# Kernel optimization log

Measured on AMD Instinct MI355X. Metric: run time of the kernel, lower is better.

Reference implementation:

```python
import jax, jax.numpy as jnp
import numpy as np

H = 4      # num_heads
C = 64     # attention_num_c
C_Z = 128  # num_in_c (pair rep channels)
C_T = 64   # num_in_c_kv (template pair channels)


def setup_inputs() -> dict:
    key = jax.random.key(0)
    ks = jax.random.split(key, 7)
    B, T, R = 1, 4, 384
    z2d = jax.random.normal(ks[0], (B, R, R, C_Z), dtype=jnp.float32)
    t2d = jax.random.normal(ks[1], (B, T, R, R, C_T), dtype=jnp.float32)
    s = 0.02
    Wq = jax.random.normal(ks[2], (C_Z, H * C), dtype=jnp.float32) * s
    Wk = jax.random.normal(ks[3], (C_T, H * C), dtype=jnp.float32) * s
    Wv = jax.random.normal(ks[4], (C_T, H * C), dtype=jnp.float32) * s
    Wo = jax.random.normal(ks[5], (H * C, C_Z), dtype=jnp.float32) * s
    bo = jax.random.normal(ks[6], (C_Z,), dtype=jnp.float32) * s
    return {"z2d": z2d, "t2d": t2d, "Wq": Wq, "Wk": Wk, "Wv": Wv, "Wo": Wo, "bo": bo}


def reference(z2d, t2d, Wq, Wk, Wv, Wo, bo):
    B, R = z2d.shape[0], z2d.shape[-2]
    T = t2d.shape[1]
    P = R * R  # residue-pair axis
    # query: one query per residue pair
    zq = z2d.reshape(B, P, 1, C_Z)
    # templates become the key/value axis per residue pair
    tkv = jnp.transpose(t2d, (0, 2, 3, 1, 4)).reshape(B, P, T, C_T)
    q = (zq @ Wq).reshape(B, P, 1, H, C) * (C ** -0.5)
    k = (tkv @ Wk).reshape(B, P, T, H, C)
    v = (tkv @ Wv).reshape(B, P, T, H, C)
    logits = jnp.einsum('bpqhc,bpkhc->bphqk', q, k)  # [B,P,H,1,T]
    weights = jax.nn.softmax(logits, axis=-1)
    weighted_avg = jnp.einsum('bphqk,bpkhc->bpqhc', weights, v)  # [B,P,1,H,C]
    out = weighted_avg.reshape(B, P, 1, H * C) @ Wo + bo
    return out.reshape(B, R, R, C_Z)
```

## Files before the change

### kernel.cpp

```cpp
#include <hip/hip_runtime.h>


#define R_    384
#define P_    (R_ * R_)
#define PB    16
#define NPB   512
#define NT_   18

typedef __attribute__((ext_vector_type(8))) short  short8;
typedef __attribute__((ext_vector_type(4))) float  f32x4;

union S8U { short8 s8; unsigned u[4]; };

__device__ __forceinline__ unsigned short f2bf(float f) {
  unsigned u = __float_as_uint(f);
  unsigned r = ((u >> 16) & 1u) + 0x7FFFu;
  return (unsigned short)((u + r) >> 16);
}
__device__ __forceinline__ float bf2f(unsigned short s) {
  return __uint_as_float(((unsigned)s) << 16);
}
__device__ __forceinline__ unsigned cvtpk(float lo, float hi) {
  unsigned d;
  asm("v_cvt_pk_bf16_f32 %0, %1, %2" : "=v"(d) : "v"(lo), "v"(hi));
  return d;
}
__device__ __forceinline__ int swz16(int p, int c) {
  return p * 256 + ((((c >> 3) ^ p) << 3) | (c & 7));
}
#define SB() __builtin_amdgcn_sched_barrier(0)
#define BAR() do { \
    asm volatile("s_waitcnt lgkmcnt(0)\ns_barrier" ::: "memory"); \
    SB(); \
  } while (0)

__device__ __forceinline__ void dma16(const float* g, void* lds) {
  __builtin_amdgcn_global_load_lds((const __attribute__((address_space(1))) unsigned*)g,
                                   (__attribute__((address_space(3))) unsigned*)lds,
                                   16, 0, 0);
}

__global__ void prep_kernel(const float* __restrict__ Wq, const float* __restrict__ Wk,
                            const float* __restrict__ Wv, const float* __restrict__ Wo,
                            unsigned short* __restrict__ AbarT,
                            unsigned short* __restrict__ MbarT) {
  int tid = blockIdx.x * blockDim.x + threadIdx.x;
  if (tid < 256 * 128) {
    int n = tid >> 7, i = tid & 127;
    int h = n >> 6, j = n & 63;
    const float* wq = Wq + i * 256 + h * 64;
    const float* wk = Wk + j * 256 + h * 64;
    float acc = 0.f;
#pragma unroll 8
    for (int c = 0; c < 64; ++c) acc += wq[c] * wk[c];
    AbarT[n * 128 + i] = f2bf(acc * 0.125f);
  } else {
    int t2 = tid - 256 * 128;
    int o = t2 >> 8, k = t2 & 255;
    int h = k >> 6, j = k & 63;
    const float* wv = Wv + j * 256 + h * 64;
    const float* wo = Wo + (h * 64) * 128 + o;
    float acc = 0.f;
#pragma unroll 8
    for (int c = 0; c < 64; ++c) acc += wv[c] * wo[c * 128];
    MbarT[o * 256 + k] = f2bf(acc);
  }
}

__global__ __launch_bounds__(256, 2) void attn_kernel(
    const float* __restrict__ z2d, const float* __restrict__ t2d,
    const unsigned short* __restrict__ AbarT, const unsigned short* __restrict__ MbarT,
    const float* __restrict__ bo, float* __restrict__ out) {
  extern __shared__ char smem[];
  float*          sTf = (float*)smem;
  unsigned short* sG  = (unsigned short*)(smem + 65536);

  const int tid  = threadIdx.x;
  const int ng   = tid >> 6;
  const int lane = tid & 63;
  const int l = lane & 15;
  const int q = lane >> 4;

  short8 ab[4][4];
#pragma unroll
  for (int kk = 0; kk < 4; ++kk)
#pragma unroll
    for (int i = 0; i < 4; ++i)
      ab[kk][i] = *(const short8*)(AbarT + ((ng * 4 + i) * 16 + l) * 128 + kk * 32 + q * 8);
  short8 mb0[8], mb1[8];
#pragma unroll
  for (int kk = 0; kk < 8; ++kk) {
    mb0[kk] = *(const short8*)(MbarT + (size_t)((ng * 2) * 16 + l) * 256 + kk * 32 + q * 8);
    mb1[kk] = *(const short8*)(MbarT + (size_t)((ng * 2 + 1) * 16 + l) * 256 + kk * 32 + q * 8);
  }
  const float bo0 = bo[ng * 32 + l];
  const float bo1 = bo[ng * 32 + 16 + l];
  SB();

#pragma unroll
  for (int s = 0; s < 3; ++s) {
    const size_t P0s = (size_t)(blockIdx.x + s * NPB) * PB;
    char* dst = (char*)sTf + s * 16384 + ng * 4096;
#pragma unroll
    for (int m = 0; m < 4; ++m) {
      const int dp  = m * 4 + q;
      const int dcf = (l ^ (((m & 1) << 2) | q)) << 2;
      dma16(t2d + ((size_t)ng * P_ + P0s + dp) * 64 + dcf, dst + m * 1024);
    }
  }
  SB();
  float4 zb[8];
  {
    const float* zr = z2d + ((size_t)blockIdx.x * PB + l) * 128;
#pragma unroll
    for (int kk = 0; kk < 4; ++kk) {
      zb[2 * kk]     = *(const float4*)(zr + kk * 32 + q * 8);
      zb[2 * kk + 1] = *(const float4*)(zr + kk * 32 + q * 8 + 4);
    }
  }
  SB();
  asm volatile("s_waitcnt vmcnt(8)" ::: "memory");
  SB();
  BAR();

#pragma unroll 1
  for (int k = 0; k < NT_; ++k) {
    const size_t P0 = (size_t)(blockIdx.x + (size_t)k * NPB) * PB;

    if (k > 0) {
      const unsigned short* sGp = sG + ((k - 1) & 1) * 4096;
      f32x4 a20 = f32x4{0.f, 0.f, 0.f, 0.f};
      f32x4 a21 = f32x4{0.f, 0.f, 0.f, 0.f};
#pragma unroll
      for (int kk = 0; kk < 8; ++kk) {
        short8 af2 = *(const short8*)(sGp + l * 256 + (((kk * 4 + q) ^ l) << 3));
        a20 = __builtin_amdgcn_mfma_f32_16x16x32_bf16(af2, mb0[kk], a20, 0, 0, 0);
        a21 = __builtin_amdgcn_mfma_f32_16x16x32_bf16(af2, mb1[kk], a21, 0, 0, 0);
      }
      const size_t rb = ((size_t)(blockIdx.x + (size_t)(k - 1) * NPB) * PB + q * 4) * 128;
#pragma unroll
      for (int r = 0; r < 4; ++r) {
        out[rb + r * 128 + ng * 32 + l]      = a20[r] + bo0;
        out[rb + r * 128 + ng * 32 + 16 + l] = a21[r] + bo1;
      }
    }
    SB();
    {
      f32x4 a1[4];
#pragma unroll
      for (int i = 0; i < 4; ++i) a1[i] = f32x4{0.f, 0.f, 0.f, 0.f};
#pragma unroll
      for (int kk = 0; kk < 4; ++kk) {
        S8U af;
        af.u[0] = cvtpk(zb[2 * kk].x,     zb[2 * kk].y);
        af.u[1] = cvtpk(zb[2 * kk].z,     zb[2 * kk].w);
        af.u[2] = cvtpk(zb[2 * kk + 1].x, zb[2 * kk + 1].y);
        af.u[3] = cvtpk(zb[2 * kk + 1].z, zb[2 * kk + 1].w);
#pragma unroll
        for (int i = 0; i < 4; ++i)
          a1[i] = __builtin_amdgcn_mfma_f32_16x16x32_bf16(af.s8, ab[kk][i], a1[i], 0, 0, 0);
      }
      unsigned short* sGc = sG + (k & 1) * 4096;
#pragma unroll
      for (int i = 0; i < 4; ++i) {
        const int c = ng * 64 + i * 16 + l;
#pragma unroll
        for (int r = 0; r < 4; ++r)
          sGc[swz16(q * 4 + r, c)] = f2bf(a1[i][r]);
      }
    }
    SB();
    if (k + 1 < NT_) {
      const float* zr = z2d + (P0 + (size_t)NPB * PB + l) * 128;
#pragma unroll
      for (int kk = 0; kk < 4; ++kk) {
        zb[2 * kk]     = *(const float4*)(zr + kk * 32 + q * 8);
        zb[2 * kk + 1] = *(const float4*)(zr + kk * 32 + q * 8 + 4);
      }
    }
    SB();
    asm volatile("s_waitcnt lgkmcnt(0)" ::: "memory");
    SB();
    {
      const float* Kt = sTf + (k & 3) * 4096;
      unsigned short* sGc = sG + (k & 1) * 4096;
      short8 g0 = *(const short8*)(sGc + swz16(l, ng * 64 + q * 16));
      short8 g1 = *(const short8*)(sGc + swz16(l, ng * 64 + q * 16 + 8));
      int aoK[4];
#pragma unroll
      for (int j = 0; j < 4; ++j)
        aoK[j] = l * 64 + (((q * 4 + j) ^ (l & 7)) << 2);
      float lg0 = 0.f, lg1 = 0.f, lg2 = 0.f, lg3 = 0.f;
#pragma unroll
      for (int j = 0; j < 4; ++j) {
        const float ga = bf2f((unsigned short)((j < 2) ? g0[4 * j]     : g1[4 * (j - 2)]));
        const float gb = bf2f((unsigned short)((j < 2) ? g0[4 * j + 1] : g1[4 * (j - 2) + 1]));
        const float gc = bf2f((unsigned short)((j < 2) ? g0[4 * j + 2] : g1[4 * (j - 2) + 2]));
        const float gd = bf2f((unsigned short)((j < 2) ? g0[4 * j + 3] : g1[4 * (j - 2) + 3]));
        float4 k0 = *(const float4*)(Kt +        aoK[j]);
        float4 k1 = *(const float4*)(Kt + 1024 + aoK[j]);
        float4 k2 = *(const float4*)(Kt + 2048 + aoK[j]);
        float4 k3 = *(const float4*)(Kt + 3072 + aoK[j]);
        lg0 += ga * k0.x + gb * k0.y + gc * k0.z + gd * k0.w;
        lg1 += ga * k1.x + gb * k1.y + gc * k1.z + gd * k1.w;
        lg2 += ga * k2.x + gb * k2.y + gc * k2.z + gd * k2.w;
        lg3 += ga * k3.x + gb * k3.y + gc * k3.z + gd * k3.w;
      }
      lg0 += __shfl_xor(lg0, 16); lg0 += __shfl_xor(lg0, 32);
      lg1 += __shfl_xor(lg1, 16); lg1 += __shfl_xor(lg1, 32);
      lg2 += __shfl_xor(lg2, 16); lg2 += __shfl_xor(lg2, 32);
      lg3 += __shfl_xor(lg3, 16); lg3 += __shfl_xor(lg3, 32);
      const float mx = fmaxf(fmaxf(lg0, lg1), fmaxf(lg2, lg3));
      float e0 = __expf(lg0 - mx), e1 = __expf(lg1 - mx);
      float e2 = __expf(lg2 - mx), e3 = __expf(lg3 - mx);
      const float inv = 1.f / (e0 + e1 + e2 + e3);
      e0 *= inv; e1 *= inv; e2 *= inv; e3 *= inv;
      asm volatile("" ::: "memory");
#pragma unroll
      for (int j = 0; j < 4; ++j) {
        float4 k0 = *(const float4*)(Kt +        aoK[j]);
        float4 k1 = *(const float4*)(Kt + 1024 + aoK[j]);
        float4 k2 = *(const float4*)(Kt + 2048 + aoK[j]);
        float4 k3 = *(const float4*)(Kt + 3072 + aoK[j]);
        float s0 = e0 * k0.x + e1 * k1.x + e2 * k2.x + e3 * k3.x;
        float s1 = e0 * k0.y + e1 * k1.y + e2 * k2.y + e3 * k3.y;
        float s2 = e0 * k0.z + e1 * k1.z + e2 * k2.z + e3 * k3.z;
        float s3 = e0 * k0.w + e1 * k1.w + e2 * k2.w + e3 * k3.w;
        uint2 w2; w2.x = cvtpk(s0, s1); w2.y = cvtpk(s2, s3);
        *(uint2*)(sGc + swz16(l, ng * 64 + q * 16 + 4 * j)) = w2;
      }
    }
    SB();
    if (k + 3 < NT_) {
      const size_t P03 = P0 + 3 * (size_t)NPB * PB;
      char* dst = (char*)sTf + ((k + 3) & 3) * 16384 + ng * 4096;
#pragma unroll
      for (int m = 0; m < 4; ++m) {
        const int dp  = m * 4 + q;
        const int dcf = (l ^ (((m & 1) << 2) | q)) << 2;
        dma16(t2d + ((size_t)ng * P_ + P03 + dp) * 64 + dcf, dst + m * 1024);
      }
    }
    SB();
    BAR();
  }

  {
    const unsigned short* sGp = sG + ((NT_ - 1) & 1) * 4096;
    f32x4 a20 = f32x4{0.f, 0.f, 0.f, 0.f};
    f32x4 a21 = f32x4{0.f, 0.f, 0.f, 0.f};
#pragma unroll
    for (int kk = 0; kk < 8; ++kk) {
      short8 af2 = *(const short8*)(sGp + l * 256 + (((kk * 4 + q) ^ l) << 3));
      a20 = __builtin_amdgcn_mfma_f32_16x16x32_bf16(af2, mb0[kk], a20, 0, 0, 0);
      a21 = __builtin_amdgcn_mfma_f32_16x16x32_bf16(af2, mb1[kk], a21, 0, 0, 0);
    }
    const size_t rb = ((size_t)(blockIdx.x + (size_t)(NT_ - 1) * NPB) * PB + q * 4) * 128;
#pragma unroll
    for (int r = 0; r < 4; ++r) {
      out[rb + r * 128 + ng * 32 + l]      = a20[r] + bo0;
      out[rb + r * 128 + ng * 32 + 16 + l] = a21[r] + bo1;
    }
  }
}

extern "C" void kernel_launch(void* const* d_in, const int* in_sizes, int n_in,
                              void* d_out, int out_size, void* d_ws, size_t ws_size,
                              hipStream_t stream) {
  const float* z2d = (const float*)d_in[0];
  const float* t2d = (const float*)d_in[1];
  const float* Wq  = (const float*)d_in[2];
  const float* Wk  = (const float*)d_in[3];
  const float* Wv  = (const float*)d_in[4];
  const float* Wo  = (const float*)d_in[5];
  const float* bo  = (const float*)d_in[6];

  unsigned short* AbarT = (unsigned short*)d_ws;
  unsigned short* MbarT = AbarT + 256 * 128;
  float* out = (float*)d_out;

  static bool attr_set = false;
  if (!attr_set) {
    (void)hipFuncSetAttribute((const void*)attn_kernel,
                              hipFuncAttributeMaxDynamicSharedMemorySize, 81920);
    attr_set = true;
  }

  hipLaunchKernelGGL(prep_kernel, dim3(256), dim3(256), 0, stream,
                     Wq, Wk, Wv, Wo, AbarT, MbarT);
  hipLaunchKernelGGL(attn_kernel, dim3(NPB), dim3(256), 81920, stream,
                     z2d, t2d, AbarT, MbarT, bo, out);
}
```

Before: 304.7 us.

## Double pair tile to 32 with 512-thread blocks and per-wave head split

Each block now handles 32 residue pairs using 8 waves, split by M-tile and head. Each wave keeps only one 16-column slice of the output-projection weights in registers, which cuts register pressure. The template stream now uses a 3-slot LDS ring (up from 4 slots) with 2-tile prefetch issued earlier in the iteration, and LDS use grows to 144 KB. Softmax switches to exp2 with log2(e) folded into the query-key weight product. The risk is that the larger LDS footprint and doubled block size limit occupancy to one block per CU, with fewer blocks in flight to hide latency.

```diff
diff --git a/kernel.cpp b/kernel.cpp
--- a/kernel.cpp
+++ b/kernel.cpp
@@ -3,8 +3,8 @@
 
 #define R_    384
 #define P_    (R_ * R_)
-#define PB    16
-#define NPB   512
+#define PB    32
+#define NPB   256
 #define NT_   18
 
 typedef __attribute__((ext_vector_type(8))) short  short8;
@@ -24,9 +24,6 @@
   unsigned d;
   asm("v_cvt_pk_bf16_f32 %0, %1, %2" : "=v"(d) : "v"(lo), "v"(hi));
   return d;
-}
-__device__ __forceinline__ int swz16(int p, int c) {
-  return p * 256 + ((((c >> 3) ^ p) << 3) | (c & 7));
 }
 #define SB() __builtin_amdgcn_sched_barrier(0)
 #define BAR() do { \
@@ -53,7 +50,7 @@
     float acc = 0.f;
 #pragma unroll 8
     for (int c = 0; c < 64; ++c) acc += wq[c] * wk[c];
-    AbarT[n * 128 + i] = f2bf(acc * 0.125f);
+    AbarT[n * 128 + i] = f2bf(acc * (0.125f * 1.44269504088896f));
   } else {
     int t2 = tid - 256 * 128;
     int o = t2 >> 8, k = t2 & 255;
@@ -67,51 +64,62 @@
   }
 }
 
-__global__ __launch_bounds__(256, 2) void attn_kernel(
+__global__ __launch_bounds__(512, 2) void attn_kernel(
     const float* __restrict__ z2d, const float* __restrict__ t2d,
     const unsigned short* __restrict__ AbarT, const unsigned short* __restrict__ MbarT,
     const float* __restrict__ bo, float* __restrict__ out) {
   extern __shared__ char smem[];
   float*          sTf = (float*)smem;
-  unsigned short* sG  = (unsigned short*)(smem + 65536);
+  unsigned short* sS  = (unsigned short*)(smem + 98304);
+  unsigned short* sGw = (unsigned short*)(smem + 131072);
 
   const int tid  = threadIdx.x;
-  const int ng   = tid >> 6;
+  const int wv_  = tid >> 6;
   const int lane = tid & 63;
   const int l = lane & 15;
   const int q = lane >> 4;
+  const int mt = wv_ & 1;
+  const int hh = wv_ >> 1;
+
+  const int pr = mt * 16 + l;
 
   short8 ab[4][4];
 #pragma unroll
   for (int kk = 0; kk < 4; ++kk)
 #pragma unroll
     for (int i = 0; i < 4; ++i)
-      ab[kk][i] = *(const short8*)(AbarT + ((ng * 4 + i) * 16 + l) * 128 + kk * 32 + q * 8);
-  short8 mb0[8], mb1[8];
-#pragma unroll
-  for (int kk = 0; kk < 8; ++kk) {
-    mb0[kk] = *(const short8*)(MbarT + (size_t)((ng * 2) * 16 + l) * 256 + kk * 32 + q * 8);
-    mb1[kk] = *(const short8*)(MbarT + (size_t)((ng * 2 + 1) * 16 + l) * 256 + kk * 32 + q * 8);
-  }
-  const float bo0 = bo[ng * 32 + l];
-  const float bo1 = bo[ng * 32 + 16 + l];
+      ab[kk][i] = *(const short8*)(AbarT + (hh * 64 + i * 16 + l) * 128 + kk * 32 + q * 8);
+  short8 mb[8];
+#pragma unroll
+  for (int kk = 0; kk < 8; ++kk)
+    mb[kk] = *(const short8*)(MbarT + (size_t)(wv_ * 16 + l) * 256 + kk * 32 + q * 8);
+  const float boR = bo[wv_ * 16 + l];
   SB();
 
-#pragma unroll
-  for (int s = 0; s < 3; ++s) {
-    const size_t P0s = (size_t)(blockIdx.x + s * NPB) * PB;
-    char* dst = (char*)sTf + s * 16384 + ng * 4096;
-#pragma unroll
-    for (int m = 0; m < 4; ++m) {
-      const int dp  = m * 4 + q;
-      const int dcf = (l ^ (((m & 1) << 2) | q)) << 2;
-      dma16(t2d + ((size_t)ng * P_ + P0s + dp) * 64 + dcf, dst + m * 1024);
-    }
+  size_t soff[4];
+#pragma unroll
+  for (int m = 0; m < 4; ++m) {
+    const int R = wv_ * 16 + m * 4 + q;
+    soff[m] = ((size_t)(R >> 5) * P_ + (R & 31)) * 64 + ((l ^ (R & 7)) << 2);
+  }
+  int aoT[4];
+#pragma unroll
+  for (int j = 0; j < 4; ++j)
+    aoT[j] = pr * 64 + (((4 * q + j) ^ (pr & 7)) << 2);
+
+  const size_t P00 = (size_t)blockIdx.x * PB;
+#pragma unroll
+  for (int s = 0; s < 2; ++s) {
+    const size_t P0s64 = (P00 + (size_t)s * NPB * PB) * 64;
+    char* dst = (char*)sTf + s * 32768 + wv_ * 4096;
+#pragma unroll
+    for (int m = 0; m < 4; ++m)
+      dma16(t2d + P0s64 + soff[m], dst + m * 1024);
   }
   SB();
   float4 zb[8];
   {
-    const float* zr = z2d + ((size_t)blockIdx.x * PB + l) * 128;
+    const float* zr = z2d + (P00 + pr) * 128;
 #pragma unroll
     for (int kk = 0; kk < 4; ++kk) {
       zb[2 * kk]     = *(const float4*)(zr + kk * 32 + q * 8);
@@ -119,29 +127,32 @@
     }
   }
   SB();
-  asm volatile("s_waitcnt vmcnt(8)" ::: "memory");
+  asm volatile("s_waitcnt vmcnt(8)\ns_barrier" ::: "memory");
   SB();
-  BAR();
 
 #pragma unroll 1
   for (int k = 0; k < NT_; ++k) {
-    const size_t P0 = (size_t)(blockIdx.x + (size_t)k * NPB) * PB;
+    const int slT = k % 3;
+    const int slG = k & 1;
+    const size_t P0 = P00 + (size_t)k * NPB * PB;
 
     if (k > 0) {
-      const unsigned short* sGp = sG + ((k - 1) & 1) * 4096;
+      const unsigned short* sSp = sS + (slG ^ 1) * 8192;
       f32x4 a20 = f32x4{0.f, 0.f, 0.f, 0.f};
       f32x4 a21 = f32x4{0.f, 0.f, 0.f, 0.f};
 #pragma unroll
       for (int kk = 0; kk < 8; ++kk) {
-        short8 af2 = *(const short8*)(sGp + l * 256 + (((kk * 4 + q) ^ l) << 3));
-        a20 = __builtin_amdgcn_mfma_f32_16x16x32_bf16(af2, mb0[kk], a20, 0, 0, 0);
-        a21 = __builtin_amdgcn_mfma_f32_16x16x32_bf16(af2, mb1[kk], a21, 0, 0, 0);
-      }
-      const size_t rb = ((size_t)(blockIdx.x + (size_t)(k - 1) * NPB) * PB + q * 4) * 128;
+        const int r0 = l, r1 = 16 + l;
+        short8 af0 = *(const short8*)(sSp + r0 * 256 + (((kk * 4 + q) ^ r0) << 3));
+        short8 af1 = *(const short8*)(sSp + r1 * 256 + (((kk * 4 + q) ^ (r1 & 31)) << 3));
+        a20 = __builtin_amdgcn_mfma_f32_16x16x32_bf16(af0, mb[kk], a20, 0, 0, 0);
+        a21 = __builtin_amdgcn_mfma_f32_16x16x32_bf16(af1, mb[kk], a21, 0, 0, 0);
+      }
+      const size_t P0p = P0 - (size_t)NPB * PB;
 #pragma unroll
       for (int r = 0; r < 4; ++r) {
-        out[rb + r * 128 + ng * 32 + l]      = a20[r] + bo0;
-        out[rb + r * 128 + ng * 32 + 16 + l] = a21[r] + bo1;
+        out[(P0p + q * 4 + r) * 128 + wv_ * 16 + l]      = a20[r] + boR;
+        out[(P0p + 16 + q * 4 + r) * 128 + wv_ * 16 + l] = a21[r] + boR;
       }
     }
     SB();
@@ -160,18 +171,28 @@
         for (int i = 0; i < 4; ++i)
           a1[i] = __builtin_amdgcn_mfma_f32_16x16x32_bf16(af.s8, ab[kk][i], a1[i], 0, 0, 0);
       }
-      unsigned short* sGc = sG + (k & 1) * 4096;
+      unsigned short* gw = sGw + wv_ * 1024;
 #pragma unroll
       for (int i = 0; i < 4; ++i) {
-        const int c = ng * 64 + i * 16 + l;
-#pragma unroll
-        for (int r = 0; r < 4; ++r)
-          sGc[swz16(q * 4 + r, c)] = f2bf(a1[i][r]);
-      }
+#pragma unroll
+        for (int r = 0; r < 4; ++r) {
+          const int row = q * 4 + r;
+          gw[row * 64 + (((2 * i + (l >> 3)) ^ (row & 7)) << 3) + (l & 7)]
+              = f2bf(a1[i][r]);
+        }
+      }
+    }
+    SB();
+    if (k + 2 < NT_) {
+      const size_t P0264 = (P0 + 2 * (size_t)NPB * PB) * 64;
+      char* dst = (char*)sTf + ((k + 2) % 3) * 32768 + wv_ * 4096;
+#pragma unroll
+      for (int m = 0; m < 4; ++m)
+        dma16(t2d + P0264 + soff[m], dst + m * 1024);
     }
     SB();
     if (k + 1 < NT_) {
-      const float* zr = z2d + (P0 + (size_t)NPB * PB + l) * 128;
+      const float* zr = z2d + (P0 + (size_t)NPB * PB + pr) * 128;
 #pragma unroll
       for (int kk = 0; kk < 4; ++kk) {
         zb[2 * kk]     = *(const float4*)(zr + kk * 32 + q * 8);
@@ -182,25 +203,25 @@
     asm volatile("s_waitcnt lgkmcnt(0)" ::: "memory");
     SB();
     {
-      const float* Kt = sTf + (k & 3) * 4096;
-      unsigned short* sGc = sG + (k & 1) * 4096;
-      short8 g0 = *(const short8*)(sGc + swz16(l, ng * 64 + q * 16));
-      short8 g1 = *(const short8*)(sGc + swz16(l, ng * 64 + q * 16 + 8));
-      int aoK[4];
-#pragma unroll
-      for (int j = 0; j < 4; ++j)
-        aoK[j] = l * 64 + (((q * 4 + j) ^ (l & 7)) << 2);
+      const float* Kt = sTf + slT * 8192;
+      const unsigned short* gw = sGw + wv_ * 1024;
+      short8 g0 = *(const short8*)(gw + l * 64 + (((2 * q) ^ (l & 7)) << 3));
+      short8 g1 = *(const short8*)(gw + l * 64 + (((2 * q + 1) ^ (l & 7)) << 3));
+      float gk[16];
+#pragma unroll
+      for (int e = 0; e < 8; ++e) {
+        gk[e]     = bf2f((unsigned short)g0[e]);
+        gk[8 + e] = bf2f((unsigned short)g1[e]);
+      }
       float lg0 = 0.f, lg1 = 0.f, lg2 = 0.f, lg3 = 0.f;
 #pragma unroll
       for (int j = 0; j < 4; ++j) {
-        const float ga = bf2f((unsigned short)((j < 2) ? g0[4 * j]     : g1[4 * (j - 2)]));
-        const float gb = bf2f((unsigned short)((j < 2) ? g0[4 * j + 1] : g1[4 * (j - 2) + 1]));
-        const float gc = bf2f((unsigned short)((j < 2) ? g0[4 * j + 2] : g1[4 * (j - 2) + 2]));
-        const float gd = bf2f((unsigned short)((j < 2) ? g0[4 * j + 3] : g1[4 * (j - 2) + 3]));
-        float4 k0 = *(const float4*)(Kt +        aoK[j]);
-        float4 k1 = *(const float4*)(Kt + 1024 + aoK[j]);
-        float4 k2 = *(const float4*)(Kt + 2048 + aoK[j]);
-        float4 k3 = *(const float4*)(Kt + 3072 + aoK[j]);
+        float4 k0 = *(const float4*)(Kt +        aoT[j]);
+        float4 k1 = *(const float4*)(Kt + 2048 + aoT[j]);
+        float4 k2 = *(const float4*)(Kt + 4096 + aoT[j]);
+        float4 k3 = *(const float4*)(Kt + 6144 + aoT[j]);
+        const float ga = gk[4 * j], gb = gk[4 * j + 1];
+        const float gc = gk[4 * j + 2], gd = gk[4 * j + 3];
         lg0 += ga * k0.x + gb * k0.y + gc * k0.z + gd * k0.w;
         lg1 += ga * k1.x + gb * k1.y + gc * k1.z + gd * k1.w;
         lg2 += ga * k2.x + gb * k2.y + gc * k2.z + gd * k2.w;
@@ -211,55 +232,47 @@
       lg2 += __shfl_xor(lg2, 16); lg2 += __shfl_xor(lg2, 32);
       lg3 += __shfl_xor(lg3, 16); lg3 += __shfl_xor(lg3, 32);
       const float mx = fmaxf(fmaxf(lg0, lg1), fmaxf(lg2, lg3));
-      float e0 = __expf(lg0 - mx), e1 = __expf(lg1 - mx);
-      float e2 = __expf(lg2 - mx), e3 = __expf(lg3 - mx);
+      float e0 = exp2f(lg0 - mx), e1 = exp2f(lg1 - mx);
+      float e2 = exp2f(lg2 - mx), e3 = exp2f(lg3 - mx);
       const float inv = 1.f / (e0 + e1 + e2 + e3);
       e0 *= inv; e1 *= inv; e2 *= inv; e3 *= inv;
       asm volatile("" ::: "memory");
+      unsigned short* sSc = sS + slG * 8192;
 #pragma unroll
       for (int j = 0; j < 4; ++j) {
-        float4 k0 = *(const float4*)(Kt +        aoK[j]);
-        float4 k1 = *(const float4*)(Kt + 1024 + aoK[j]);
-        float4 k2 = *(const float4*)(Kt + 2048 + aoK[j]);
-        float4 k3 = *(const float4*)(Kt + 3072 + aoK[j]);
+        float4 k0 = *(const float4*)(Kt +        aoT[j]);
+        float4 k1 = *(const float4*)(Kt + 2048 + aoT[j]);
+        float4 k2 = *(const float4*)(Kt + 4096 + aoT[j]);
+        float4 k3 = *(const float4*)(Kt + 6144 + aoT[j]);
         float s0 = e0 * k0.x + e1 * k1.x + e2 * k2.x + e3 * k3.x;
         float s1 = e0 * k0.y + e1 * k1.y + e2 * k2.y + e3 * k3.y;
         float s2 = e0 * k0.z + e1 * k1.z + e2 * k2.z + e3 * k3.z;
         float s3 = e0 * k0.w + e1 * k1.w + e2 * k2.w + e3 * k3.w;
+        const int c = hh * 64 + q * 16 + j * 4;
         uint2 w2; w2.x = cvtpk(s0, s1); w2.y = cvtpk(s2, s3);
-        *(uint2*)(sGc + swz16(l, ng * 64 + q * 16 + 4 * j)) = w2;
-      }
-    }
-    SB();
-    if (k + 3 < NT_) {
-      const size_t P03 = P0 + 3 * (size_t)NPB * PB;
-      char* dst = (char*)sTf + ((k + 3) & 3) * 16384 + ng * 4096;
-#pragma unroll
-      for (int m = 0; m < 4; ++m) {
-        const int dp  = m * 4 + q;
-        const int dcf = (l ^ (((m & 1) << 2) | q)) << 2;
-        dma16(t2d + ((size_t)ng * P_ + P03 + dp) * 64 + dcf, dst + m * 1024);
-      }
-    }
-    SB();
+        *(uint2*)(sSc + pr * 256 + ((((c >> 3) ^ (pr & 31)) << 3) | (c & 7))) = w2;
+      }
+    }
     BAR();
   }
 
   {
-    const unsigned short* sGp = sG + ((NT_ - 1) & 1) * 4096;
+    const unsigned short* sSp = sS + 8192;
     f32x4 a20 = f32x4{0.f, 0.f, 0.f, 0.f};
     f32x4 a21 = f32x4{0.f, 0.f, 0.f, 0.f};
 #pragma unroll
     for (int kk = 0; kk < 8; ++kk) {
-      short8 af2 = *(const short8*)(sGp + l * 256 + (((kk * 4 + q) ^ l) << 3));
-      a20 = __builtin_amdgcn_mfma_f32_16x16x32_bf16(af2, mb0[kk], a20, 0, 0, 0);
-      a21 = __builtin_amdgcn_mfma_f32_16x16x32_bf16(af2, mb1[kk], a21, 0, 0, 0);
-    }
-    const size_t rb = ((size_t)(blockIdx.x + (size_t)(NT_ - 1) * NPB) * PB + q * 4) * 128;
+      const int r0 = l, r1 = 16 + l;
+      short8 af0 = *(const short8*)(sSp + r0 * 256 + (((kk * 4 + q) ^ r0) << 3));
+      short8 af1 = *(const short8*)(sSp + r1 * 256 + (((kk * 4 + q) ^ (r1 & 31)) << 3));
+      a20 = __builtin_amdgcn_mfma_f32_16x16x32_bf16(af0, mb[kk], a20, 0, 0, 0);
+      a21 = __builtin_amdgcn_mfma_f32_16x16x32_bf16(af1, mb[kk], a21, 0, 0, 0);
+    }
+    const size_t P0p = P00 + (size_t)(NT_ - 1) * NPB * PB;
 #pragma unroll
     for (int r = 0; r < 4; ++r) {
-      out[rb + r * 128 + ng * 32 + l]      = a20[r] + bo0;
-      out[rb + r * 128 + ng * 32 + 16 + l] = a21[r] + bo1;
+      out[(P0p + q * 4 + r) * 128 + wv_ * 16 + l]      = a20[r] + boR;
+      out[(P0p + 16 + q * 4 + r) * 128 + wv_ * 16 + l] = a21[r] + boR;
     }
   }
 }
@@ -282,12 +295,12 @@
   static bool attr_set = false;
   if (!attr_set) {
     (void)hipFuncSetAttribute((const void*)attn_kernel,
-                              hipFuncAttributeMaxDynamicSharedMemorySize, 81920);
+                              hipFuncAttributeMaxDynamicSharedMemorySize, 147456);
     attr_set = true;
   }
 
   hipLaunchKernelGGL(prep_kernel, dim3(256), dim3(256), 0, stream,
                      Wq, Wk, Wv, Wo, AbarT, MbarT);
-  hipLaunchKernelGGL(attn_kernel, dim3(NPB), dim3(256), 81920, stream,
+  hipLaunchKernelGGL(attn_kernel, dim3(NPB), dim3(512), 147456, stream,
                      z2d, t2d, AbarT, MbarT, bo, out);
 }
```

New measurement: 316.6 us. 3.9% more time.
